# Kernel tuning notes

Measured on AMD Instinct MI355X. Metric: run time of the kernel, lower is better.

The kernel has to match this reference:

```python
import jax, jax.numpy as jnp
import numpy as np


def setup_inputs() -> dict:
    key = jax.random.key(0)
    k1, k2, k3, k4, k5 = jax.random.split(key, 5)
    B, Tq, Tk, Q, K, U = 8, 32, 2048, 256, 256, 256
    s = 1.0 / np.sqrt(U)
    return {
        "query": jax.random.normal(k1, (B, Tq, Q), dtype=jnp.float32),
        "keys": jax.random.normal(k2, (B, Tk, K), dtype=jnp.float32),
        "Wq": jax.random.normal(k3, (U, Q), dtype=jnp.float32) * s,
        "Wk": jax.random.normal(k4, (U, K), dtype=jnp.float32) * s,
        "v": jax.random.normal(k5, (U,), dtype=jnp.float32) * s,
    }


def reference(query, keys, Wq, Wk, v):
    # Bahdanau additive attention (batch_first, normalize=False)
    # q_proj: [B, Tq, U], k_proj: [B, Tk, U]
    q_proj = jnp.einsum("bqd,ud->bqu", query, Wq)
    k_proj = jnp.einsum("bkd,ud->bku", keys, Wk)
    # additive score: tanh(q + k) . v -> [B, Tq, Tk]
    sum_qk = jnp.tanh(q_proj[:, :, None, :] + k_proj[:, None, :, :])
    scores = jnp.einsum("bqku,u->bqk", sum_qk, v)
    attn = jax.nn.softmax(scores, axis=-1)  # over encoder time Tk
    # weighted sum of encoder states (keys double as values, as in GNMT)
    context = jnp.einsum("bqk,bkd->bqd", attn, keys)
    return context, attn
```

## Files before the change

kernel.cpp:

```cpp
#include <hip/hip_runtime.h>
#include <hip/hip_bf16.h>

#define SCALE_2LOG2E 2.8853900817779268f
#define LOG2E 1.4426950408889634f

#define NB 8
#define TQ 32
#define TK 2048
#define DD 256

typedef unsigned short u16;
typedef u16 u16x8 __attribute__((ext_vector_type(8)));
typedef __bf16 bf16x8 __attribute__((ext_vector_type(8)));
typedef float f32x4 __attribute__((ext_vector_type(4)));

__device__ __forceinline__ u16 f2bf_u(float x) {
  unsigned int xi = __builtin_bit_cast(unsigned int, x);
  unsigned int r = (xi + 0x7fffu + ((xi >> 16) & 1u)) >> 16;
  return (u16)r;
}
__device__ __forceinline__ float bf2f(u16 u) {
  return __builtin_bit_cast(float, (unsigned int)u << 16);
}

__global__ __launch_bounds__(256) void convert_kernel(
    const float* __restrict__ Wk, const float* __restrict__ Wq,
    u16* __restrict__ wkh, u16* __restrict__ wkl,
    u16* __restrict__ wqh, u16* __restrict__ wql) {
  const int bx = blockIdx.x;
  const float* src; u16 *dh, *dl; int base;
  if (bx < 32) { src = Wk; dh = wkh; dl = wkl; base = 0; }
  else         { src = Wq; dh = wqh; dl = wql; base = 32; }
  const int chunk = (bx - base) * 256 + threadIdx.x;
  const float4* s4 = (const float4*)(src + chunk * 8);
  float4 x0 = s4[0], x1 = s4[1];
  const float xs[8] = {x0.x, x0.y, x0.z, x0.w, x1.x, x1.y, x1.z, x1.w};
  u16x8 h, l;
#pragma unroll
  for (int i = 0; i < 8; ++i) {
    u16 hh = f2bf_u(xs[i]);
    h[i] = hh;
    l[i] = f2bf_u(xs[i] - bf2f(hh));
  }
  *(u16x8*)(dh + chunk * 8) = h;
  *(u16x8*)(dl + chunk * 8) = l;
}

__global__ __launch_bounds__(512) void proj_fused(
    const float* __restrict__ keys, const float* __restrict__ query,
    const u16* __restrict__ wkh, const u16* __restrict__ wkl,
    const u16* __restrict__ wqh, const u16* __restrict__ wql,
    float* __restrict__ ekpo, float* __restrict__ eqpo) {
  __shared__ u16 Ah[64 * 64], Al[64 * 64];
  __shared__ u16 Bh[256 * 64], Bl[256 * 64];
  const int tid = threadIdx.x, lane = tid & 63, wv = tid >> 6;
  const int bx = blockIdx.x;
  const float* A; const u16 *bhg, *blg; float* C; int m0;
  if (bx < 256) { A = keys;  bhg = wkh; blg = wkl; C = ekpo; m0 = bx * 64; }
  else          { A = query; bhg = wqh; blg = wql; C = eqpo; m0 = (bx - 256) * 64; }
  const int wr = (wv >> 2) * 32, wc = (wv & 3) * 64;

  const int arow = tid >> 3, ac = tid & 7;
  const float* ag = A + (m0 + arow) * 256 + ac * 8;
  const int aoff = arow * 64 + ((ac ^ (arow & 7)) << 3);

  f32x4 acc[2][4];
#pragma unroll
  for (int i = 0; i < 2; ++i)
#pragma unroll
    for (int j = 0; j < 4; ++j) acc[i][j] = {0.f, 0.f, 0.f, 0.f};

  for (int ks = 0; ks < 4; ++ks) {
    const int k0 = ks * 64;
    float4 a0 = *(const float4*)(ag + k0);
    float4 a1 = *(const float4*)(ag + k0 + 4);
    u16x8 sbh[4], sbl[4];
    int boff[4];
#pragma unroll
    for (int j = 0; j < 4; ++j) {
      int idx = tid + j * 512;
      int row = idx >> 3, c = idx & 7;
      sbh[j] = *(const u16x8*)(bhg + row * 256 + k0 + c * 8);
      sbl[j] = *(const u16x8*)(blg + row * 256 + k0 + c * 8);
      boff[j] = row * 64 + ((c ^ (row & 7)) << 3);
    }
    const float as[8] = {a0.x, a0.y, a0.z, a0.w, a1.x, a1.y, a1.z, a1.w};
    u16x8 hA, lA;
#pragma unroll
    for (int i = 0; i < 8; ++i) {
      u16 hh = f2bf_u(as[i]);
      hA[i] = hh;
      lA[i] = f2bf_u(as[i] - bf2f(hh));
    }
    if (ks) __syncthreads();
    *(u16x8*)&Ah[aoff] = hA;
    *(u16x8*)&Al[aoff] = lA;
#pragma unroll
    for (int j = 0; j < 4; ++j) {
      *(u16x8*)&Bh[boff[j]] = sbh[j];
      *(u16x8*)&Bl[boff[j]] = sbl[j];
    }
    __syncthreads();
#pragma unroll
    for (int s = 0; s < 2; ++s) {
      const int kc = s * 4 + (lane >> 4);
      bf16x8 fa[2][2], fb[4][2];
#pragma unroll
      for (int mh = 0; mh < 2; ++mh) {
        int ra = wr + mh * 16 + (lane & 15);
        int off = ra * 64 + ((kc ^ (ra & 7)) << 3);
        fa[mh][0] = __builtin_bit_cast(bf16x8, *(const u16x8*)&Ah[off]);
        fa[mh][1] = __builtin_bit_cast(bf16x8, *(const u16x8*)&Al[off]);
      }
#pragma unroll
      for (int nh = 0; nh < 4; ++nh) {
        int rb = wc + nh * 16 + (lane & 15);
        int off = rb * 64 + ((kc ^ (rb & 7)) << 3);
        fb[nh][0] = __builtin_bit_cast(bf16x8, *(const u16x8*)&Bh[off]);
        fb[nh][1] = __builtin_bit_cast(bf16x8, *(const u16x8*)&Bl[off]);
      }
#pragma unroll
      for (int mh = 0; mh < 2; ++mh)
#pragma unroll
        for (int nh = 0; nh < 4; ++nh) {
          acc[mh][nh] = __builtin_amdgcn_mfma_f32_16x16x32_bf16(fa[mh][0], fb[nh][0], acc[mh][nh], 0, 0, 0);
          acc[mh][nh] = __builtin_amdgcn_mfma_f32_16x16x32_bf16(fa[mh][0], fb[nh][1], acc[mh][nh], 0, 0, 0);
          acc[mh][nh] = __builtin_amdgcn_mfma_f32_16x16x32_bf16(fa[mh][1], fb[nh][0], acc[mh][nh], 0, 0, 0);
        }
    }
  }
#pragma unroll
  for (int mh = 0; mh < 2; ++mh)
#pragma unroll
    for (int nh = 0; nh < 4; ++nh)
#pragma unroll
      for (int j = 0; j < 4; ++j) {
        int row = m0 + wr + mh * 16 + (lane >> 4) * 4 + j;
        int col = wc + nh * 16 + (lane & 15);
        C[row * 256 + col] = __builtin_amdgcn_exp2f(acc[mh][nh][j] * SCALE_2LOG2E);
      }
}

__global__ __launch_bounds__(512) void score_ctx_kernel(
    const float* __restrict__ ekp, const float* __restrict__ eqp,
    const float* __restrict__ v, const float* __restrict__ keys,
    float* __restrict__ pbuf, float* __restrict__ part) {
  __shared__ float sbuf[64 * 256];
  __shared__ float eqlds[16 * 256];
  const int tid = threadIdx.x;
  const int b = blockIdx.y;
  const int kc = blockIdx.x;
  const int qh = blockIdx.z;
  const int kbase = kc * 64;
#pragma unroll
  for (int i = 0; i < 8; ++i) {
    int idx4 = tid + i * 512;
    int kk = idx4 >> 6, u4 = idx4 & 63;
    float4 t = *(const float4*)(ekp + (b * TK + kbase + kk) * 256 + u4 * 4);
    *(float4*)&sbuf[kk * 256 + ((u4 ^ (kk & 7)) << 2)] = t;
  }
#pragma unroll
  for (int i = 0; i < 2; ++i) {
    int idx4 = tid + i * 512;
    int r = idx4 >> 6, u4 = idx4 & 63;
    float4 t = *(const float4*)(eqp + (b * TQ + qh * 16 + r) * 256 + u4 * 4);
    *(float4*)&eqlds[r * 256 + u4 * 4] = t;
  }
  const int lane = tid & 63;
  float vs = (v[lane] + v[lane + 64]) + (v[lane + 128] + v[lane + 192]);
#pragma unroll
  for (int off = 32; off; off >>= 1) vs += __shfl_xor(vs, off, 64);
  __syncthreads();

  const int wv = tid >> 6;
  const int q0 = qh * 16 + wv * 2;
  const int xorv = lane & 7;
  const float* eq0 = &eqlds[(wv * 2) * 256];
  const float* eq1 = eq0 + 256;
  float a00 = 0.f, a01 = 0.f, a10 = 0.f, a11 = 0.f;
#pragma unroll 4
  for (int u4 = 0; u4 < 64; ++u4) {
    float4 ekv = *(const float4*)&sbuf[lane * 256 + ((u4 ^ xorv) << 2)];
    float4 qa = *(const float4*)(eq0 + u4 * 4);
    float4 qb = *(const float4*)(eq1 + u4 * 4);
    float4 vv = *(const float4*)(v + u4 * 4);
    float A0 = fmaf(ekv.x, qa.x, 1.f);
    float A1 = fmaf(ekv.y, qa.y, 1.f);
    float A2 = fmaf(ekv.z, qa.z, 1.f);
    float A3 = fmaf(ekv.w, qa.w, 1.f);
    float n01 = fmaf(vv.x, A1, vv.y * A0);
    float n23 = fmaf(vv.z, A3, vv.w * A2);
    a00 = fmaf(n01, __builtin_amdgcn_rcpf(A0 * A1), a00);
    a01 = fmaf(n23, __builtin_amdgcn_rcpf(A2 * A3), a01);
    float B0 = fmaf(ekv.x, qb.x, 1.f);
    float B1 = fmaf(ekv.y, qb.y, 1.f);
    float B2 = fmaf(ekv.z, qb.z, 1.f);
    float B3 = fmaf(ekv.w, qb.w, 1.f);
    float m01 = fmaf(vv.x, B1, vv.y * B0);
    float m23 = fmaf(vv.z, B3, vv.w * B2);
    a10 = fmaf(m01, __builtin_amdgcn_rcpf(B0 * B1), a10);
    a11 = fmaf(m23, __builtin_amdgcn_rcpf(B2 * B3), a11);
  }
  float sc0 = fmaf(-2.f, a00 + a01, vs);
  float sc1 = fmaf(-2.f, a10 + a11, vs);
  float p0 = __builtin_amdgcn_exp2f(sc0 * LOG2E);
  float p1 = __builtin_amdgcn_exp2f(sc1 * LOG2E);
  const int row0 = b * TQ + q0;
  pbuf[row0 * TK + kbase + lane] = p0;
  pbuf[(row0 + 1) * TK + kbase + lane] = p1;

  __syncthreads();
#pragma unroll
  for (int i = 0; i < 8; ++i) {
    int idx4 = tid + i * 512;
    int kk = idx4 >> 6, d4 = idx4 & 63;
    float4 kv = *(const float4*)(keys + (b * TK + kbase + kk) * 256 + d4 * 4);
    *(float4*)&sbuf[kk * 256 + d4 * 4] = kv;
  }
  __syncthreads();

  float4 o0 = {0.f, 0.f, 0.f, 0.f}, o1 = {0.f, 0.f, 0.f, 0.f};
  const int ip0 = __builtin_bit_cast(int, p0);
  const int ip1 = __builtin_bit_cast(int, p1);
#pragma unroll 8
  for (int k = 0; k < 64; ++k) {
    float4 kv = *(const float4*)&sbuf[k * 256 + lane * 4];
    float pk0 = __builtin_bit_cast(float, __builtin_amdgcn_readlane(ip0, k));
    float pk1 = __builtin_bit_cast(float, __builtin_amdgcn_readlane(ip1, k));
    o0.x = fmaf(pk0, kv.x, o0.x); o0.y = fmaf(pk0, kv.y, o0.y);
    o0.z = fmaf(pk0, kv.z, o0.z); o0.w = fmaf(pk0, kv.w, o0.w);
    o1.x = fmaf(pk1, kv.x, o1.x); o1.y = fmaf(pk1, kv.y, o1.y);
    o1.z = fmaf(pk1, kv.z, o1.z); o1.w = fmaf(pk1, kv.w, o1.w);
  }
  float* prow = part + (b * 32 + kc) * 8192 + q0 * 256 + lane * 4;
  *(float4*)prow = o0;
  *(float4*)(prow + 256) = o1;
}

__global__ __launch_bounds__(256) void combine_kernel(
    const float* __restrict__ part, const float* __restrict__ pbuf,
    float* __restrict__ ctx, float* __restrict__ attn) {
  const int row = blockIdx.x;
  const int b = row >> 5, q = row & 31;
  const int tid = threadIdx.x;
  const float4* p4 = (const float4*)(pbuf + row * TK);
  float4 x0 = p4[tid], x1 = p4[tid + 256];
  float s = ((x0.x + x0.y) + (x0.z + x0.w)) + ((x1.x + x1.y) + (x1.z + x1.w));
#pragma unroll
  for (int off = 32; off; off >>= 1) s += __shfl_xor(s, off, 64);
  __shared__ float reds[4];
  __shared__ float sInvL;
  const int lane = tid & 63, wv = tid >> 6;
  if (lane == 0) reds[wv] = s;
  __syncthreads();
  if (tid == 0) {
    float L = (reds[0] + reds[1]) + (reds[2] + reds[3]);
    sInvL = __builtin_amdgcn_rcpf(L);
  }
  __syncthreads();
  const float invL = sInvL;
  float4* a4 = (float4*)(attn + row * TK);
  a4[tid] = make_float4(x0.x * invL, x0.y * invL, x0.z * invL, x0.w * invL);
  a4[tid + 256] = make_float4(x1.x * invL, x1.y * invL, x1.z * invL, x1.w * invL);
  const float* p = part + b * 32 * 8192 + q * 256 + tid;
  float c0 = 0.f, c1 = 0.f, c2 = 0.f, c3 = 0.f;
#pragma unroll
  for (int kc = 0; kc < 8; ++kc) {
    c0 += p[(kc * 4 + 0) * 8192];
    c1 += p[(kc * 4 + 1) * 8192];
    c2 += p[(kc * 4 + 2) * 8192];
    c3 += p[(kc * 4 + 3) * 8192];
  }
  ctx[row * 256 + tid] = ((c0 + c1) + (c2 + c3)) * invL;
}

extern "C" void kernel_launch(void* const* d_in, const int* in_sizes, int n_in,
                              void* d_out, int out_size, void* d_ws, size_t ws_size,
                              hipStream_t stream) {
  const float* query = (const float*)d_in[0];
  const float* keys  = (const float*)d_in[1];
  const float* Wq    = (const float*)d_in[2];
  const float* Wk    = (const float*)d_in[3];
  const float* v     = (const float*)d_in[4];

  float* out  = (float*)d_out;
  float* ctx  = out;
  float* attn = out + 65536;

  float* ws   = (float*)d_ws;
  float* ekp  = ws;
  float* eqp  = ws + 4194304;
  float* pbuf = ws + 4259840;
  float* part = ws + 4784128;
  u16* u   = (u16*)(ws + 6881280);
  u16* wkh = u;
  u16* wkl = wkh + 65536;
  u16* wqh = wkl + 65536;
  u16* wql = wqh + 65536;

  convert_kernel<<<64, 256, 0, stream>>>(Wk, Wq, wkh, wkl, wqh, wql);
  proj_fused<<<260, 512, 0, stream>>>(keys, query, wkh, wkl, wqh, wql, ekp, eqp);
  score_ctx_kernel<<<dim3(32, 8, 2), 512, 0, stream>>>(ekp, eqp, v, keys, pbuf, part);
  combine_kernel<<<256, 256, 0, stream>>>(part, pbuf, ctx, attn);
}
```

Measured before the change: 55.20 us.

## Pipeline ekp chunk loads and prefetch keys into registers during score loop

The single up-front load of the 64x256 ekp tile is split into four 64-column chunks. Each next chunk is loaded from global memory into registers while the current chunk is computed, then written to LDS behind a barrier. The keys tile for the context phase is prefetched into registers during the last two chunks, so its global latency overlaps the score math. This adds register pressure (8 float4 for keys plus the chunk buffers) and three extra barriers. It is coherent only because each chunk's columns match the u4 range read in that stage.

```diff
diff --git a/kernel.cpp b/kernel.cpp
--- a/kernel.cpp
+++ b/kernel.cpp
@@ -152,55 +152,92 @@
   const int kc = blockIdx.x;
   const int qh = blockIdx.z;
   const int kbase = kc * 64;
-#pragma unroll
-  for (int i = 0; i < 8; ++i) {
-    int idx4 = tid + i * 512;
-    int kk = idx4 >> 6, u4 = idx4 & 63;
-    float4 t = *(const float4*)(ekp + (b * TK + kbase + kk) * 256 + u4 * 4);
-    *(float4*)&sbuf[kk * 256 + ((u4 ^ (kk & 7)) << 2)] = t;
-  }
-#pragma unroll
-  for (int i = 0; i < 2; ++i) {
-    int idx4 = tid + i * 512;
-    int r = idx4 >> 6, u4 = idx4 & 63;
-    float4 t = *(const float4*)(eqp + (b * TQ + qh * 16 + r) * 256 + u4 * 4);
-    *(float4*)&eqlds[r * 256 + u4 * 4] = t;
-  }
   const int lane = tid & 63;
-  float vs = (v[lane] + v[lane + 64]) + (v[lane + 128] + v[lane + 192]);
-#pragma unroll
-  for (int off = 32; off; off >>= 1) vs += __shfl_xor(vs, off, 64);
-  __syncthreads();
-
   const int wv = tid >> 6;
   const int q0 = qh * 16 + wv * 2;
+
+  const int kk0 = tid >> 4, c0 = tid & 15;
+  const int kk1 = (tid + 512) >> 4, c1 = tid & 15;
+  const float* ekrow0 = ekp + (b * TK + kbase + kk0) * 256;
+  const float* ekrow1 = ekp + (b * TK + kbase + kk1) * 256;
+  const int eoff0 = kk0 * 256 + (((c0) ^ (kk0 & 7)) << 2);
+  const int eoff1 = kk1 * 256 + (((c1) ^ (kk1 & 7)) << 2);
+
+  float4 e0 = *(const float4*)(ekrow0 + c0 * 4);
+  float4 e1 = *(const float4*)(ekrow1 + c1 * 4);
+  const int eqr0 = tid >> 6, equ0 = tid & 63;
+  const int eqr1 = (tid + 512) >> 6, equ1 = tid & 63;
+  float4 q0v = *(const float4*)(eqp + (b * TQ + qh * 16 + eqr0) * 256 + equ0 * 4);
+  float4 q1v = *(const float4*)(eqp + (b * TQ + qh * 16 + eqr1) * 256 + equ1 * 4);
+  float vs = (v[lane] + v[lane + 64]) + (v[lane + 128] + v[lane + 192]);
+#pragma unroll
+  for (int off = 32; off; off >>= 1) vs += __shfl_xor(vs, off, 64);
+  *(float4*)&sbuf[kk0 * 256 + ((c0 ^ (kk0 & 7)) << 2)] = e0;
+  *(float4*)&sbuf[kk1 * 256 + ((c1 ^ (kk1 & 7)) << 2)] = e1;
+  *(float4*)&eqlds[eqr0 * 256 + equ0 * 4] = q0v;
+  *(float4*)&eqlds[eqr1 * 256 + equ1 * 4] = q1v;
+  __syncthreads();
+
   const int xorv = lane & 7;
   const float* eq0 = &eqlds[(wv * 2) * 256];
   const float* eq1 = eq0 + 256;
   float a00 = 0.f, a01 = 0.f, a10 = 0.f, a11 = 0.f;
+  float4 pk[8];
+
+#pragma unroll
+  for (int s = 0; s < 4; ++s) {
+    float4 n0, n1;
+    if (s < 3) {
+      n0 = *(const float4*)(ekrow0 + ((s + 1) * 16 + c0) * 4);
+      n1 = *(const float4*)(ekrow1 + ((s + 1) * 16 + c1) * 4);
+    }
+    if (s == 2) {
+#pragma unroll
+      for (int j = 0; j < 4; ++j) {
+        int idx = tid + j * 512;
+        pk[j] = *(const float4*)(keys + (b * TK + kbase + (idx >> 6)) * 256 + (idx & 63) * 4);
+      }
+    }
+    if (s == 3) {
+#pragma unroll
+      for (int j = 4; j < 8; ++j) {
+        int idx = tid + j * 512;
+        pk[j] = *(const float4*)(keys + (b * TK + kbase + (idx >> 6)) * 256 + (idx & 63) * 4);
+      }
+    }
 #pragma unroll 4
-  for (int u4 = 0; u4 < 64; ++u4) {
-    float4 ekv = *(const float4*)&sbuf[lane * 256 + ((u4 ^ xorv) << 2)];
-    float4 qa = *(const float4*)(eq0 + u4 * 4);
-    float4 qb = *(const float4*)(eq1 + u4 * 4);
-    float4 vv = *(const float4*)(v + u4 * 4);
-    float A0 = fmaf(ekv.x, qa.x, 1.f);
-    float A1 = fmaf(ekv.y, qa.y, 1.f);
-    float A2 = fmaf(ekv.z, qa.z, 1.f);
-    float A3 = fmaf(ekv.w, qa.w, 1.f);
-    float n01 = fmaf(vv.x, A1, vv.y * A0);
-    float n23 = fmaf(vv.z, A3, vv.w * A2);
-    a00 = fmaf(n01, __builtin_amdgcn_rcpf(A0 * A1), a00);
-    a01 = fmaf(n23, __builtin_amdgcn_rcpf(A2 * A3), a01);
-    float B0 = fmaf(ekv.x, qb.x, 1.f);
-    float B1 = fmaf(ekv.y, qb.y, 1.f);
-    float B2 = fmaf(ekv.z, qb.z, 1.f);
-    float B3 = fmaf(ekv.w, qb.w, 1.f);
-    float m01 = fmaf(vv.x, B1, vv.y * B0);
-    float m23 = fmaf(vv.z, B3, vv.w * B2);
-    a10 = fmaf(m01, __builtin_amdgcn_rcpf(B0 * B1), a10);
-    a11 = fmaf(m23, __builtin_amdgcn_rcpf(B2 * B3), a11);
-  }
+    for (int t = 0; t < 16; ++t) {
+      const int u4 = s * 16 + t;
+      float4 ekv = *(const float4*)&sbuf[lane * 256 + ((u4 ^ xorv) << 2)];
+      float4 qa = *(const float4*)(eq0 + u4 * 4);
+      float4 qb = *(const float4*)(eq1 + u4 * 4);
+      float4 vv = *(const float4*)(v + u4 * 4);
+      float A0 = fmaf(ekv.x, qa.x, 1.f);
+      float A1 = fmaf(ekv.y, qa.y, 1.f);
+      float A2 = fmaf(ekv.z, qa.z, 1.f);
+      float A3 = fmaf(ekv.w, qa.w, 1.f);
+      float n01 = fmaf(vv.x, A1, vv.y * A0);
+      float n23 = fmaf(vv.z, A3, vv.w * A2);
+      a00 = fmaf(n01, __builtin_amdgcn_rcpf(A0 * A1), a00);
+      a01 = fmaf(n23, __builtin_amdgcn_rcpf(A2 * A3), a01);
+      float B0 = fmaf(ekv.x, qb.x, 1.f);
+      float B1 = fmaf(ekv.y, qb.y, 1.f);
+      float B2 = fmaf(ekv.z, qb.z, 1.f);
+      float B3 = fmaf(ekv.w, qb.w, 1.f);
+      float m01 = fmaf(vv.x, B1, vv.y * B0);
+      float m23 = fmaf(vv.z, B3, vv.w * B2);
+      a10 = fmaf(m01, __builtin_amdgcn_rcpf(B0 * B1), a10);
+      a11 = fmaf(m23, __builtin_amdgcn_rcpf(B2 * B3), a11);
+    }
+    if (s < 3) {
+      const int u4n0 = (s + 1) * 16 + c0;
+      const int u4n1 = (s + 1) * 16 + c1;
+      *(float4*)&sbuf[kk0 * 256 + ((u4n0 ^ (kk0 & 7)) << 2)] = n0;
+      *(float4*)&sbuf[kk1 * 256 + ((u4n1 ^ (kk1 & 7)) << 2)] = n1;
+      __syncthreads();
+    }
+  }
+
   float sc0 = fmaf(-2.f, a00 + a01, vs);
   float sc1 = fmaf(-2.f, a10 + a11, vs);
   float p0 = __builtin_amdgcn_exp2f(sc0 * LOG2E);
@@ -211,11 +248,9 @@
 
   __syncthreads();
 #pragma unroll
-  for (int i = 0; i < 8; ++i) {
-    int idx4 = tid + i * 512;
-    int kk = idx4 >> 6, d4 = idx4 & 63;
-    float4 kv = *(const float4*)(keys + (b * TK + kbase + kk) * 256 + d4 * 4);
-    *(float4*)&sbuf[kk * 256 + d4 * 4] = kv;
+  for (int j = 0; j < 8; ++j) {
+    int idx = tid + j * 512;
+    *(float4*)&sbuf[(idx >> 6) * 256 + (idx & 63) * 4] = pk[j];
   }
   __syncthreads();
 
```

Result: slower. 62.05 us (+12.4%).
